# Performance work log

Measured on AMD Instinct MI355X. Metric: run time of the kernel, lower is better.

Reference implementation:

```python
import jax, jax.numpy as jnp
import numpy as np

HEADS, DH, M, ITERS = 8, 64, 256, 6
DIM = 512


def layer_norm(x, g, b, eps=1e-5):
    mu = x.mean(-1, keepdims=True)
    var = x.var(-1, keepdims=True)
    return (x - mu) / jnp.sqrt(var + eps) * g + b


def moore_penrose_pinv(x, iters=ITERS):
    abs_x = jnp.abs(x)
    col = abs_x.sum(-1)
    row = abs_x.sum(-2)
    z = jnp.swapaxes(x, -1, -2) / (jnp.max(col) * jnp.max(row))
    I = jnp.eye(x.shape[-1], dtype=x.dtype)
    for _ in range(iters):
        xz = x @ z
        z = 0.25 * z @ (13.0 * I - xz @ (15.0 * I - xz @ (7.0 * I - xz)))
    return z


def nystrom_attn(x, w_qkv, w_out, b_out, res_w):
    b, n, _ = x.shape
    pad = (M - n % M) % M
    xp = jnp.pad(x, ((0, 0), (pad, 0), (0, 0)))  # left-pad seq as in lucidrains
    npad = n + pad
    l = npad // M  # == ceil(n / M)
    qkv = xp @ w_qkv
    q, k, v = jnp.split(qkv, 3, axis=-1)
    to_heads = lambda t: t.reshape(b, npad, HEADS, DH).transpose(0, 2, 1, 3)
    q, k, v = to_heads(q), to_heads(k), to_heads(v)
    q = q * (DH ** -0.5)
    # landmarks: mean over consecutive chunks of size l  ('(n l) d -> n d')
    ql = q.reshape(b, HEADS, M, l, DH).mean(3)
    kl = k.reshape(b, HEADS, M, l, DH).mean(3)
    a1 = jax.nn.softmax(jnp.einsum('bhid,bhjd->bhij', q, kl), -1)   # (b,h,npad,M)
    a2 = jax.nn.softmax(jnp.einsum('bhid,bhjd->bhij', ql, kl), -1)  # (b,h,M,M)
    a3 = jax.nn.softmax(jnp.einsum('bhid,bhjd->bhij', ql, k), -1)   # (b,h,M,npad)
    a2inv = moore_penrose_pinv(a2)
    out = a1 @ (a2inv @ (a3 @ v))  # (b,h,npad,DH)
    # residual depthwise conv along sequence, per head (kernel (33,1), groups=heads)
    res = jax.lax.conv_general_dilated(v, res_w, window_strides=(1, 1),
                                       padding=((16, 16), (0, 0)),
                                       dimension_numbers=('NCHW', 'OIHW', 'NCHW'),
                                       feature_group_count=HEADS)
    out = out + res
    out = out.transpose(0, 2, 1, 3).reshape(b, npad, HEADS * DH)
    out = out @ w_out + b_out
    return out[:, -n:]


def ppeg(x, w7, b7, w5, b5, w3, b3, Hh, Ww):
    B, n, C = x.shape
    cls_tok, feat = x[:, :1], x[:, 1:]
    cnn = feat.transpose(0, 2, 1).reshape(B, C, Hh, Ww)

    def dwconv(w, bb, p):
        y = jax.lax.conv_general_dilated(cnn, w, (1, 1), ((p, p), (p, p)),
                                         dimension_numbers=('NCHW', 'OIHW', 'NCHW'),
                                         feature_group_count=C)
        return y + bb[None, :, None, None]

    y = cnn + dwconv(w7, b7, 3) + dwconv(w5, b5, 2) + dwconv(w3, b3, 1)
    y = y.reshape(B, C, Hh * Ww).transpose(0, 2, 1)
    return jnp.concatenate([cls_tok, y], axis=1)


def setup_inputs() -> dict:
    key = jax.random.key(0)
    ks = iter(jax.random.split(key, 32))
    rn = lambda shape, s=0.02: jax.random.normal(next(ks), shape, dtype=jnp.float32) * s
    inp = {
        'data': jax.random.normal(next(ks), (1, 16000, 1024), dtype=jnp.float32),
        'fc1_w': rn((1024, 512)), 'fc1_b': jnp.zeros((512,), jnp.float32),
        'cls_token': rn((1, 1, 512), 1.0),
        'l1_norm_g': jnp.ones((512,), jnp.float32), 'l1_norm_b': jnp.zeros((512,), jnp.float32),
        'l1_qkv_w': rn((512, 1536)), 'l1_out_w': rn((512, 512)), 'l1_out_b': jnp.zeros((512,), jnp.float32),
        'l1_res_w': rn((8, 1, 33, 1)),
        'ppeg_w7': rn((512, 1, 7, 7)), 'ppeg_b7': jnp.zeros((512,), jnp.float32),
        'ppeg_w5': rn((512, 1, 5, 5)), 'ppeg_b5': jnp.zeros((512,), jnp.float32),
        'ppeg_w3': rn((512, 1, 3, 3)), 'ppeg_b3': jnp.zeros((512,), jnp.float32),
        'l2_norm_g': jnp.ones((512,), jnp.float32), 'l2_norm_b': jnp.zeros((512,), jnp.float32),
        'l2_qkv_w': rn((512, 1536)), 'l2_out_w': rn((512, 512)), 'l2_out_b': jnp.zeros((512,), jnp.float32),
        'l2_res_w': rn((8, 1, 33, 1)),
        'norm_g': jnp.ones((512,), jnp.float32), 'norm_b': jnp.zeros((512,), jnp.float32),
        'fc2_w': rn((512, 2)), 'fc2_b': jnp.zeros((2,), jnp.float32),
    }
    return inp


def reference(data, fc1_w, fc1_b, cls_token, l1_norm_g, l1_norm_b, l1_qkv_w, l1_out_w,
              l1_out_b, l1_res_w, ppeg_w7, ppeg_b7, ppeg_w5, ppeg_b5, ppeg_w3, ppeg_b3,
              l2_norm_g, l2_norm_b, l2_qkv_w, l2_out_w, l2_out_b, l2_res_w,
              norm_g, norm_b, fc2_w, fc2_b):
    h = jax.nn.relu(data @ fc1_w + fc1_b)  # (B, N, 512)
    N = h.shape[1]
    s = int(np.ceil(np.sqrt(N)))  # square grid side
    add = s * s - N
    h = jnp.concatenate([h, h[:, :add]], axis=1)  # repeat-pad to s*s
    B = h.shape[0]
    cls = jnp.broadcast_to(cls_token, (B, 1, h.shape[2]))
    h = jnp.concatenate([cls, h], axis=1)  # (B, s*s+1, 512)
    h = h + nystrom_attn(layer_norm(h, l1_norm_g, l1_norm_b), l1_qkv_w, l1_out_w, l1_out_b, l1_res_w)
    h = ppeg(h, ppeg_w7, ppeg_b7, ppeg_w5, ppeg_b5, ppeg_w3, ppeg_b3, s, s)
    h = h + nystrom_attn(layer_norm(h, l2_norm_g, l2_norm_b), l2_qkv_w, l2_out_w, l2_out_b, l2_res_w)
    h = layer_norm(h, norm_g, norm_b)[:, 0]
    logits = h @ fc2_w + fc2_b
    Y_prob = jax.nn.softmax(logits, -1)
    Y_hat = jnp.argmax(logits, -1)
    return logits, Y_prob, Y_hat
```

## Files before the change

### kernel.cpp

```cpp
#include <hip/hip_runtime.h>
#include <math.h>

#define NPAD   16384
#define PADR   254
#define NTOK   16130
#define NPIX   16129
#define SG     127
#define DD     512
#define NH     8
#define CHK    64

typedef __attribute__((ext_vector_type(8))) short bf16x8;
typedef __attribute__((ext_vector_type(4))) float f32x4;

__device__ __forceinline__ ushort f2bf(float f) {
  uint u = __float_as_uint(f);
  u = (u + 0x7fffu + ((u >> 16) & 1u)) >> 16;
  return (ushort)u;
}

__global__ __launch_bounds__(256) void cvt_bf_kernel(
    const float* __restrict__ src, ushort* __restrict__ dst, int n)
{
  int i = (blockIdx.x * 256 + threadIdx.x) * 8;
// ... 42 lines not shown
#pragma unroll
    for (int j = 0; j < 4; ++j) acc[i][j] = (f32x4){0.f, 0.f, 0.f, 0.f};

  for (int k0 = 0; k0 < K; k0 += 64) {
    __syncthreads();
#pragma unroll
    for (int i = 0; i < 4; ++i) {
      int id = t + i * 256;
      int r = id >> 3, blk = id & 7;
      int gr = m0 + r;
      bf16x8 v = (bf16x8){0, 0, 0, 0, 0, 0, 0, 0};
      if (gr < M) v = *(const bf16x8*)(A + (size_t)gr * lda + k0 + blk * 8);
      *(bf16x8*)(As + r * 64 + ((blk ^ (r & 7)) << 3)) = v;
    }
#pragma unroll
    for (int i = 0; i < 4; ++i) {
      int id = t + i * 256;
      int r = id >> 3, blk = id & 7;
      bf16x8 v = *(const bf16x8*)(Bt + (size_t)(n0 + r) * ldb + k0 + blk * 8);
      *(bf16x8*)(Bs + r * 64 + ((blk ^ (r & 7)) << 3)) = v;
    }
    __syncthreads();
    bf16x8 af[4][2], bfr[4][2];
#pragma unroll
    for (int rt = 0; rt < 4; ++rt) {
      int row = wr * 64 + rt * 16 + lr;
#pragma unroll
      for (int kc = 0; kc < 2; ++kc)
        af[rt][kc] = *(const bf16x8*)(As + row * 64 + (((kc * 4 + lg) ^ (row & 7)) << 3));
    }
#pragma unroll
    for (int nt = 0; nt < 4; ++nt) {
      int row = wc * 64 + nt * 16 + lr;
#pragma unroll
      for (int kc = 0; kc < 2; ++kc)
        bfr[nt][kc] = *(const bf16x8*)(Bs + row * 64 + (((kc * 4 + lg) ^ (row & 7)) << 3));
    }
#pragma unroll
    for (int rt = 0; rt < 4; ++rt)
#pragma unroll
      for (int nt = 0; nt < 4; ++nt) {
        acc[rt][nt] = __builtin_amdgcn_mfma_f32_16x16x32_bf16(af[rt][0], bfr[nt][0], acc[rt][nt], 0, 0, 0);
        acc[rt][nt] = __builtin_amdgcn_mfma_f32_16x16x32_bf16(af[rt][1], bfr[nt][1], acc[rt][nt], 0, 0, 0);
      }
  }
#pragma unroll
  for (int rt = 0; rt < 4; ++rt) {
#pragma unroll
    for (int r = 0; r < 4; ++r) {
      int gi = m0 + wr * 64 + rt * 16 + lg * 4 + r;
      if (gi >= M) continue;
#pragma unroll
      for (int nt = 0; nt < 4; ++nt) {
        int gj = n0 + wc * 64 + nt * 16 + lr;
        float d = acc[rt][nt][r];
        if (mode == 1) d = fmaxf(d + bias[gj], 0.f);
        else if (mode == 2) { if (gj < 512) d *= 0.125f; }
        else if (mode == 3) d += C[(size_t)gi * ldc + gj] + bias[gj];
        C[(size_t)gi * ldc + gj] = d;
      }
    }
  }
}

__global__ __launch_bounds__(256) void gemm_bt(
    const float* __restrict__ A, int lda,
    const ushort* __restrict__ Bt, int ldb,
    float* __restrict__ C, int ldc,
    int M, int K, int mode, const float* __restrict__ bias)
{
  const int t = threadIdx.x;
  const int w = t >> 6, l = t & 63, lr = l & 15, lg = l >> 4;
  const int wr = w >> 1, wc = w & 1;
  const int m0 = blockIdx.y * 128, n0 = blockIdx.x * 128;
  __shared__ __align__(16) ushort As[128 * 64];
  __shared__ __align__(16) ushort Bs[128 * 64];
  f32x4 acc[4][4];
#pragma unroll
  for (int i = 0; i < 4; ++i)
#pragma unroll
    for (int j = 0; j < 4; ++j) acc[i][j] = (f32x4){0.f, 0.f, 0.f, 0.f};

  for (int k0 = 0; k0 < K; k0 += 64) {
    __syncthreads();
#pragma unroll
    for (int i = 0; i < 2; ++i) {
      int id = t + i * 256;
      int r = id >> 2, db = id & 3;
      const float* src = A + (size_t)(m0 + r) * lda + k0 + db * 16;
      float4 g0 = *(const float4*)(src + 0);
      float4 g1 = *(const float4*)(src + 4);
      float4 g2 = *(const float4*)(src + 8);
      float4 g3 = *(const float4*)(src + 12);
      bf16x8 e0, e1;
      e0[0] = f2bf(g0.x); e0[1] = f2bf(g0.y); e0[2] = f2bf(g0.z); e0[3] = f2bf(g0.w);
      e0[4] = f2bf(g1.x); e0[5] = f2bf(g1.y); e0[6] = f2bf(g1.z); e0[7] = f2bf(g1.w);
      e1[0] = f2bf(g2.x); e1[1] = f2bf(g2.y); e1[2] = f2bf(g2.z); e1[3] = f2bf(g2.w);
      e1[4] = f2bf(g3.x); e1[5] = f2bf(g3.y); e1[6] = f2bf(g3.z); e1[7] = f2bf(g3.w);
      ushort* dst = As + r * 64;
      *(bf16x8*)(dst + (((db * 2 + 0) ^ (r & 7)) << 3)) = e0;
      *(bf16x8*)(dst + (((db * 2 + 1) ^ (r & 7)) << 3)) = e1;
    }
#pragma unroll
    for (int i = 0; i < 4; ++i) {
      int id = t + i * 256;
      int r = id >> 3, blk = id & 7;
      bf16x8 v = *(const bf16x8*)(Bt + (size_t)(n0 + r) * ldb + k0 + blk * 8);
      *(bf16x8*)(Bs + r * 64 + ((blk ^ (r & 7)) << 3)) = v;
    }
    __syncthreads();
    bf16x8 af[4][2], bfr[4][2];
#pragma unroll
    for (int rt = 0; rt < 4; ++rt) {
      int row = wr * 64 + rt * 16 + lr;
#pragma unroll
      for (int kc = 0; kc < 2; ++kc)
        af[rt][kc] = *(const bf16x8*)(As + row * 64 + (((kc * 4 + lg) ^ (row & 7)) << 3));
    }
#pragma unroll
    for (int nt = 0; nt < 4; ++nt) {
      int row = wc * 64 + nt * 16 + lr;
#pragma unroll
      for (int kc = 0; kc < 2; ++kc)
        bfr[nt][kc] = *(const bf16x8*)(Bs + row * 64 + (((kc * 4 + lg) ^ (row & 7)) << 3));
    }
#pragma unroll
    for (int rt = 0; rt < 4; ++rt)
#pragma unroll
      for (int nt = 0; nt < 4; ++nt) {
        acc[rt][nt] = __builtin_amdgcn_mfma_f32_16x16x32_bf16(af[rt][0], bfr[nt][0], acc[rt][nt], 0, 0, 0);
        acc[rt][nt] = __builtin_amdgcn_mfma_f32_16x16x32_bf16(af[rt][1], bfr[nt][1], acc[rt][nt], 0, 0, 0);
      }
  }
#pragma unroll
  for (int rt = 0; rt < 4; ++rt) {
#pragma unroll
    for (int r = 0; r < 4; ++r) {
      int gi = m0 + wr * 64 + rt * 16 + lg * 4 + r;
      if (gi >= M) continue;
#pragma unroll
      for (int nt = 0; nt < 4; ++nt) {
        int gj = n0 + wc * 64 + nt * 16 + lr;
        float d = acc[rt][nt][r];
        if (mode == 1) d = fmaxf(d + bias[gj], 0.f);
        else if (mode == 2) { if (gj < 512) d *= 0.125f; }
        else if (mode == 3) d += C[(size_t)gi * ldc + gj] + bias[gj];
        C[(size_t)gi * ldc + gj] = d;
      }
    }
  }
}


__global__ __launch_bounds__(256) void nmm_kernel(
    const float* __restrict__ A, const float* __restrict__ B,
    float* __restrict__ C, int mode)
{
  const int h_ = blockIdx.z;
  const int m0 = blockIdx.y * 64, n0 = blockIdx.x * 64;
  const float* Ah = A + (size_t)h_ * 65536;
  const float* Bh = B + (size_t)h_ * 65536;
  float* Ch = C + (size_t)h_ * 65536;
  const int t = threadIdx.x, w = t >> 6, l = t & 63, lr = l & 15, lg = l >> 4;
  __shared__ __align__(16) ushort Xs[64 * 64];
  __shared__ __align__(16) ushort Ys[64 * 64];
  f32x4 acc[4];
#pragma unroll
  for (int nt = 0; nt < 4; ++nt) acc[nt] = (f32x4){0.f, 0.f, 0.f, 0.f};

  for (int k0 = 0; k0 < 256; k0 += 64) {
    __syncthreads();
    {
      int r = t >> 2, db = t & 3;
      const float* src = Ah + (size_t)(m0 + r) * 256 + k0 + db * 16;
      float4 g0 = *(const float4*)(src + 0);
      float4 g1 = *(const float4*)(src + 4);
      float4 g2 = *(const float4*)(src + 8);
      float4 g3 = *(const float4*)(src + 12);
      bf16x8 e0, e1;
      e0[0] = f2bf(g0.x); e0[1] = f2bf(g0.y); e0[2] = f2bf(g0.z); e0[3] = f2bf(g0.w);
      e0[4] = f2bf(g1.x); e0[5] = f2bf(g1.y); e0[6] = f2bf(g1.z); e0[7] = f2bf(g1.w);
      e1[0] = f2bf(g2.x); e1[1] = f2bf(g2.y); e1[2] = f2bf(g2.z); e1[3] = f2bf(g2.w);
      e1[4] = f2bf(g3.x); e1[5] = f2bf(g3.y); e1[6] = f2bf(g3.z); e1[7] = f2bf(g3.w);
      ushort* dst = Xs + r * 64;
      *(bf16x8*)(dst + (((db * 2 + 0) ^ (r & 7)) << 3)) = e0;
      *(bf16x8*)(dst + (((db * 2 + 1) ^ (r & 7)) << 3)) = e1;
    }
#pragma unroll
    for (int i = 0; i < 4; ++i) {
      int id = t + i * 256;
      int k = id >> 4, q = id & 15;
      float4 v = *(const float4*)(Bh + (size_t)(k0 + k) * 256 + n0 + q * 4);
      int kb = k >> 3, ke = k & 7;
      Ys[(q * 4 + 0) * 64 + ((kb ^ ((q * 4 + 0) & 7)) << 3) + ke] = f2bf(v.x);
      Ys[(q * 4 + 1) * 64 + ((kb ^ ((q * 4 + 1) & 7)) << 3) + ke] = f2bf(v.y);
      Ys[(q * 4 + 2) * 64 + ((kb ^ ((q * 4 + 2) & 7)) << 3) + ke] = f2bf(v.z);
      Ys[(q * 4 + 3) * 64 + ((kb ^ ((q * 4 + 3) & 7)) << 3) + ke] = f2bf(v.w);
    }
    __syncthreads();
    int arow = w * 16 + lr;
    bf16x8 af0 = *(const bf16x8*)(Xs + arow * 64 + (((0 + lg) ^ (arow & 7)) << 3));
    bf16x8 af1 = *(const bf16x8*)(Xs + arow * 64 + (((4 + lg) ^ (arow & 7)) << 3));
#pragma unroll
    for (int nt = 0; nt < 4; ++nt) {
      int brow = nt * 16 + lr;
      bf16x8 bf0 = *(const bf16x8*)(Ys + brow * 64 + (((0 + lg) ^ (brow & 7)) << 3));
      bf16x8 bf1 = *(const bf16x8*)(Ys + brow * 64 + (((4 + lg) ^ (brow & 7)) << 3));
      acc[nt] = __builtin_amdgcn_mfma_f32_16x16x32_bf16(af0, bf0, acc[nt], 0, 0, 0);
      acc[nt] = __builtin_amdgcn_mfma_f32_16x16x32_bf16(af1, bf1, acc[nt], 0, 0, 0);
    }
  }
#pragma unroll
  for (int nt = 0; nt < 4; ++nt) {
#pragma unroll
    for (int r = 0; r < 4; ++r) {
      int gi = m0 + w * 16 + lg * 4 + r;
      int gj = n0 + nt * 16 + lr;
      float d = acc[nt][r];
      if (mode == 1) d = 7.f * Ah[(size_t)gi * 256 + gj] - d;
      Ch[(size_t)gi * 256 + gj] = d;
    }
  }
}

__global__ __launch_bounds__(256) void nmm_s2(
    const float* __restrict__ Z, const float* __restrict__ z,
    float* __restrict__ W, float* __restrict__ G)
{
  const int h_ = blockIdx.z & 7;
  const int job = blockIdx.z >> 3;
  const int m0 = blockIdx.y * 64, n0 = blockIdx.x * 64;
  const float* Ah = Z + (size_t)h_ * 65536;
  const float* Bh = (job == 0 ? z : Z) + (size_t)h_ * 65536;
  float* Ch = (job == 0 ? W : G) + (size_t)h_ * 65536;
  const int t = threadIdx.x, w = t >> 6, l = t & 63, lr = l & 15, lg = l >> 4;
  __shared__ __align__(16) ushort Xs[64 * 64];
  __shared__ __align__(16) ushort Ys[64 * 64];
  f32x4 acc[4];
#pragma unroll
  for (int nt = 0; nt < 4; ++nt) acc[nt] = (f32x4){0.f, 0.f, 0.f, 0.f};

  for (int k0 = 0; k0 < 256; k0 += 64) {
    __syncthreads();
    {
      int r = t >> 2, db = t & 3;
      const float* src = Ah + (size_t)(m0 + r) * 256 + k0 + db * 16;
      float4 g0 = *(const float4*)(src + 0);
      float4 g1 = *(const float4*)(src + 4);
      float4 g2 = *(const float4*)(src + 8);
      float4 g3 = *(const float4*)(src + 12);
      bf16x8 e0, e1;
      e0[0] = f2bf(g0.x); e0[1] = f2bf(g0.y); e0[2] = f2bf(g0.z); e0[3] = f2bf(g0.w);
      e0[4] = f2bf(g1.x); e0[5] = f2bf(g1.y); e0[6] = f2bf(g1.z); e0[7] = f2bf(g1.w);
      e1[0] = f2bf(g2.x); e1[1] = f2bf(g2.y); e1[2] = f2bf(g2.z); e1[3] = f2bf(g2.w);
      e1[4] = f2bf(g3.x); e1[5] = f2bf(g3.y); e1[6] = f2bf(g3.z); e1[7] = f2bf(g3.w);
      ushort* dst = Xs + r * 64;
      *(bf16x8*)(dst + (((db * 2 + 0) ^ (r & 7)) << 3)) = e0;
      *(bf16x8*)(dst + (((db * 2 + 1) ^ (r & 7)) << 3)) = e1;
    }
#pragma unroll
    for (int i = 0; i < 4; ++i) {
      int id = t + i * 256;
      int k = id >> 4, q = id & 15;
      float4 v = *(const float4*)(Bh + (size_t)(k0 + k) * 256 + n0 + q * 4);
      int kb = k >> 3, ke = k & 7;
      Ys[(q * 4 + 0) * 64 + ((kb ^ ((q * 4 + 0) & 7)) << 3) + ke] = f2bf(v.x);
      Ys[(q * 4 + 1) * 64 + ((kb ^ ((q * 4 + 1) & 7)) << 3) + ke] = f2bf(v.y);
      Ys[(q * 4 + 2) * 64 + ((kb ^ ((q * 4 + 2) & 7)) << 3) + ke] = f2bf(v.z);
      Ys[(q * 4 + 3) * 64 + ((kb ^ ((q * 4 + 3) & 7)) << 3) + ke] = f2bf(v.w);
    }
    __syncthreads();
    int arow = w * 16 + lr;
    bf16x8 af0 = *(const bf16x8*)(Xs + arow * 64 + (((0 + lg) ^ (arow & 7)) << 3));
    bf16x8 af1 = *(const bf16x8*)(Xs + arow * 64 + (((4 + lg) ^ (arow & 7)) << 3));
#pragma unroll
    for (int nt = 0; nt < 4; ++nt) {
      int brow = nt * 16 + lr;
      bf16x8 bf0 = *(const bf16x8*)(Ys + brow * 64 + (((0 + lg) ^ (brow & 7)) << 3));
      bf16x8 bf1 = *(const bf16x8*)(Ys + brow * 64 + (((4 + lg) ^ (brow & 7)) << 3));
      acc[nt] = __builtin_amdgcn_mfma_f32_16x16x32_bf16(af0, bf0, acc[nt], 0, 0, 0);
      acc[nt] = __builtin_amdgcn_mfma_f32_16x16x32_bf16(af1, bf1, acc[nt], 0, 0, 0);
    }
  }
#pragma unroll
  for (int nt = 0; nt < 4; ++nt) {
#pragma unroll
    for (int r = 0; r < 4; ++r) {
      int gi = m0 + w * 16 + lg * 4 + r;
      int gj = n0 + nt * 16 + lr;
      float d = acc[nt][r];
      if (job == 1) d = 7.f * Ah[(size_t)gi * 256 + gj] - d;
      Ch[(size_t)gi * 256 + gj] = d;
    }
  }
}

__global__ __launch_bounds__(256) void nmm_s3(
    const float* __restrict__ G, const float* __restrict__ W,
    const float* __restrict__ zc, float* __restrict__ zn)
{
  const int h_ = blockIdx.z;
  const int m0 = blockIdx.y * 64, n0 = blockIdx.x * 64;
  const float* Ah = G + (size_t)h_ * 65536;
  const float* Bh = W + (size_t)h_ * 65536;
  const float* Eh = zc + (size_t)h_ * 65536;
  float* Ch = zn + (size_t)h_ * 65536;
  const int t = threadIdx.x, w = t >> 6, l = t & 63, lr = l & 15, lg = l >> 4;
  __shared__ __align__(16) ushort Xs[64 * 64];
  __shared__ __align__(16) ushort Ys[64 * 64];
  f32x4 acc[4];
#pragma unroll
  for (int nt = 0; nt < 4; ++nt) acc[nt] = (f32x4){0.f, 0.f, 0.f, 0.f};

  for (int k0 = 0; k0 < 256; k0 += 64) {
    __syncthreads();
    {
      int r = t >> 2, db = t & 3;
      const float* src = Ah + (size_t)(m0 + r) * 256 + k0 + db * 16;
      float4 g0 = *(const float4*)(src + 0);
      float4 g1 = *(const float4*)(src + 4);
      float4 g2 = *(const float4*)(src + 8);
      float4 g3 = *(const float4*)(src + 12);
      bf16x8 e0, e1;
      e0[0] = f2bf(g0.x); e0[1] = f2bf(g0.y); e0[2] = f2bf(g0.z); e0[3] = f2bf(g0.w);
      e0[4] = f2bf(g1.x); e0[5] = f2bf(g1.y); e0[6] = f2bf(g1.z); e0[7] = f2bf(g1.w);
      e1[0] = f2bf(g2.x); e1[1] = f2bf(g2.y); e1[2] = f2bf(g2.z); e1[3] = f2bf(g2.w);
      e1[4] = f2bf(g3.x); e1[5] = f2bf(g3.y); e1[6] = f2bf(g3.z); e1[7] = f2bf(g3.w);
      ushort* dst = Xs + r * 64;
      *(bf16x8*)(dst + (((db * 2 + 0) ^ (r & 7)) << 3)) = e0;
      *(bf16x8*)(dst + (((db * 2 + 1) ^ (r & 7)) << 3)) = e1;
    }
#pragma unroll
    for (int i = 0; i < 4; ++i) {
      int id = t + i * 256;
      int k = id >> 4, q = id & 15;
      float4 v = *(const float4*)(Bh + (size_t)(k0 + k) * 256 + n0 + q * 4);
      int kb = k >> 3, ke = k & 7;
      Ys[(q * 4 + 0) * 64 + ((kb ^ ((q * 4 + 0) & 7)) << 3) + ke] = f2bf(v.x);
      Ys[(q * 4 + 1) * 64 + ((kb ^ ((q * 4 + 1) & 7)) << 3) + ke] = f2bf(v.y);
      Ys[(q * 4 + 2) * 64 + ((kb ^ ((q * 4 + 2) & 7)) << 3) + ke] = f2bf(v.z);
      Ys[(q * 4 + 3) * 64 + ((kb ^ ((q * 4 + 3) & 7)) << 3) + ke] = f2bf(v.w);
    }
    __syncthreads();
    int arow = w * 16 + lr;
    bf16x8 af0 = *(const bf16x8*)(Xs + arow * 64 + (((0 + lg) ^ (arow & 7)) << 3));
    bf16x8 af1 = *(const bf16x8*)(Xs + arow * 64 + (((4 + lg) ^ (arow & 7)) << 3));
#pragma unroll
    for (int nt = 0; nt < 4; ++nt) {
      int brow = nt * 16 + lr;
      bf16x8 bf0 = *(const bf16x8*)(Ys + brow * 64 + (((0 + lg) ^ (brow & 7)) << 3));
      bf16x8 bf1 = *(const bf16x8*)(Ys + brow * 64 + (((4 + lg) ^ (brow & 7)) << 3));
      acc[nt] = __builtin_amdgcn_mfma_f32_16x16x32_bf16(af0, bf0, acc[nt], 0, 0, 0);
      acc[nt] = __builtin_amdgcn_mfma_f32_16x16x32_bf16(af1, bf1, acc[nt], 0, 0, 0);
    }
  }
#pragma unroll
  for (int nt = 0; nt < 4; ++nt) {
#pragma unroll
    for (int r = 0; r < 4; ++r) {
      int gi = m0 + w * 16 + lg * 4 + r;
      int gj = n0 + nt * 16 + lr;
      size_t o = (size_t)gi * 256 + gj;
      Ch[o] = 0.25f * (13.f * Eh[o] - 15.f * Bh[o] + acc[nt][r]);
    }
  }
}

__global__ __launch_bounds__(256) void assemble_kernel(float* __restrict__ h,
                                                       const float* __restrict__ cls)
{
  int idx = blockIdx.x * 256 + threadIdx.x;
  if (idx < 512) { h[idx] = cls[idx]; return; }
  idx -= 512;
  int i = idx >> 9, c = idx & 511;
  h[(size_t)(16001 + i) * DD + c] = h[(size_t)(1 + i) * DD + c];
}

__global__ __launch_bounds__(256) void ln_pad_kernel(
    const float* __restrict__ h, ushort* __restrict__ xn,
    const float* __restrict__ g, const float* __restrict__ b)
{
  int row = blockIdx.x;
  int t = threadIdx.x;
  if (row < PADR) {
    xn[(size_t)row * DD + t] = 0;
    xn[(size_t)row * DD + t + 256] = 0;
    return;
  }
  const float* x = h + (size_t)(row - PADR) * DD;
  __shared__ float red[256];
  float v0 = x[t], v1 = x[t + 256];
  red[t] = v0 + v1;
  __syncthreads();
  for (int s = 128; s > 0; s >>= 1) { if (t < s) red[t] += red[t + s]; __syncthreads(); }
  float mu = red[0] * (1.f / 512.f);
  __syncthreads();
  float d0 = v0 - mu, d1 = v1 - mu;
  red[t] = d0 * d0 + d1 * d1;
  __syncthreads();
  for (int s = 128; s > 0; s >>= 1) { if (t < s) red[t] += red[t + s]; __syncthreads(); }
  float rs = rsqrtf(red[0] * (1.f / 512.f) + 1e-5f);
  ushort* o = xn + (size_t)row * DD;
  o[t]       = f2bf(d0 * rs * g[t] + b[t]);
  o[t + 256] = f2bf(d1 * rs * g[t + 256] + b[t + 256]);
}

__global__ __launch_bounds__(256) void landmark_kernel(
    const float* __restrict__ qkv, float* __restrict__ ql, float* __restrict__ kl)
{
  int i = blockIdx.x;
  int c = blockIdx.y * 256 + threadIdx.x;
  const float* p = qkv + (size_t)(i * 64) * 1536 + c;
  float s = 0.f;
  for (int j = 0; j < 64; ++j) s += p[(size_t)j * 1536];
  s *= (1.f / 64.f);
  if (c < 512) ql[(size_t)i * 512 + c] = s;
  else         kl[(size_t)i * 512 + (c - 512)] = s;
}

__global__ __launch_bounds__(256) void a2_kernel(
    const float* __restrict__ ql, const float* __restrict__ kl, float* __restrict__ a2)
{
  int h_ = blockIdx.x, i = blockIdx.y;
  int t = threadIdx.x;
  __shared__ float q[64];
  __shared__ float red[256];
  if (t < 64) q[t] = ql[(size_t)i * 512 + h_ * 64 + t];
  __syncthreads();
  const float* kr = kl + (size_t)t * 512 + h_ * 64;
  float s = 0.f;
#pragma unroll
  for (int d = 0; d < 64; ++d) s = fmaf(q[d], kr[d], s);
  red[t] = s;
  __syncthreads();
  for (int st = 128; st > 0; st >>= 1) { if (t < st) red[t] = fmaxf(red[t], red[t + st]); __syncthreads(); }
  float mx = red[0];
  __syncthreads();
  float e = __expf(s - mx);
  red[t] = e;
  __syncthreads();
  for (int st = 128; st > 0; st >>= 1) { if (t < st) red[t] += red[t + st]; __syncthreads(); }
  a2[((size_t)h_ * 256 + i) * 256 + t] = e / red[0];
}

__global__ __launch_bounds__(256) void pinv_red1(const float* __restrict__ a2, float* __restrict__ red)
{
  int h_ = blockIdx.x, t = threadIdx.x;
  const float* X = a2 + (size_t)h_ * 65536;
  float rs = 0.f, cs = 0.f;
  for (int j = 0; j < 256; ++j) rs += fabsf(X[(size_t)t * 256 + j]);
  for (int i = 0; i < 256; ++i) cs += fabsf(X[(size_t)i * 256 + t]);
  __shared__ float r1[256], r2[256];
  r1[t] = rs; r2[t] = cs;
  __syncthreads();
  for (int s = 128; s > 0; s >>= 1) {
    if (t < s) { r1[t] = fmaxf(r1[t], r1[t + s]); r2[t] = fmaxf(r2[t], r2[t + s]); }
    __syncthreads();
  }
  if (t == 0) { red[h_ * 2] = r1[0]; red[h_ * 2 + 1] = r2[0]; }
}
__global__ __launch_bounds__(256) void pinv_init(
    const float* __restrict__ a2, const float* __restrict__ red, float* __restrict__ z)
{
  int h_ = blockIdx.x, i = blockIdx.y, j = threadIdx.x;
  float mr = 0.f, mc = 0.f;
#pragma unroll
  for (int k = 0; k < 8; ++k) { mr = fmaxf(mr, red[k * 2]); mc = fmaxf(mc, red[k * 2 + 1]); }
  float inv = 1.f / (mr * mc);
  z[((size_t)h_ * 256 + i) * 256 + j] = a2[((size_t)h_ * 256 + j) * 256 + i] * inv;
}

__global__ __launch_bounds__(256) void mmb_kernel(
    const float* __restrict__ A, const float* __restrict__ B, float* __restrict__ C,
    int N, float alpha)
{
  int h_ = blockIdx.z;
  const float* Ah = A + (size_t)h_ * 256 * 256;
  const float* Bh = B + (size_t)h_ * 256 * N;
  float* Ch = C + (size_t)h_ * 256 * N;
  int m0 = blockIdx.y * 64, n0 = blockIdx.x * 64;
  __shared__ float As[16][68];
  __shared__ float Bs[16][68];
  int tid = threadIdx.x, tx = tid & 15, ty = tid >> 4;
  float acc[4][4];
#pragma unroll
  for (int i = 0; i < 4; ++i)
#pragma unroll
    for (int j = 0; j < 4; ++j) acc[i][j] = 0.f;
  for (int k0 = 0; k0 < 256; k0 += 16) {
    {
      int row = tid >> 2, k4 = (tid & 3) << 2;
      float4 v = *(const float4*)(Ah + (size_t)(m0 + row) * 256 + k0 + k4);
      As[k4 + 0][row] = v.x; As[k4 + 1][row] = v.y;
      As[k4 + 2][row] = v.z; As[k4 + 3][row] = v.w;
    }
    {
      int row = tid >> 4, c4 = (tid & 15) << 2;
      *(float4*)&Bs[row][c4] = *(const float4*)(Bh + (size_t)(k0 + row) * N + n0 + c4);
    }
    __syncthreads();
#pragma unroll
    for (int k = 0; k < 16; ++k) {
      float a[4], b[4];
      *(float4*)a = *(const float4*)&As[k][ty * 4];
      *(float4*)b = *(const float4*)&Bs[k][tx * 4];
#pragma unroll
      for (int i = 0; i < 4; ++i)
#pragma unroll
        for (int j = 0; j < 4; ++j) acc[i][j] = fmaf(a[i], b[j], acc[i][j]);
    }
    __syncthreads();
  }
#pragma unroll
  for (int i = 0; i < 4; ++i) {
    float4 r;
    r.x = alpha * acc[i][0]; r.y = alpha * acc[i][1];
    r.z = alpha * acc[i][2]; r.w = alpha * acc[i][3];
    *(float4*)(Ch + (size_t)(m0 + ty * 4 + i) * N + n0 + tx * 4) = r;
  }
}

__global__ __launch_bounds__(256) void a3v_mfma(
    const float* __restrict__ qkv, const float* __restrict__ ql,
    float* __restrict__ pacc, float* __restrict__ den)
{
  const int h_ = blockIdx.x;
  const int ch = blockIdx.y;
  const int t  = threadIdx.x;
  const int w  = t >> 6;
  const int l  = t & 63;
  const int lr = l & 15;
  const int lg = l >> 4;

  __shared__ __align__(16) ushort kls[64 * 64];
  __shared__ __align__(16) ushort vls[80 * 64];
  __shared__ __align__(16) ushort pls[4][64 * 64];

  bf16x8 qf[4][2];
#pragma unroll
  for (int rt = 0; rt < 4; ++rt)
#pragma unroll
    for (int dc = 0; dc < 2; ++dc) {
      const float* p = ql + (size_t)(64 * w + rt * 16 + lr) * 512 + h_ * 64 + dc * 32 + lg * 8;
      float4 f0 = *(const float4*)p;
      float4 f1 = *(const float4*)(p + 4);
      bf16x8 v;
      v[0] = f2bf(f0.x); v[1] = f2bf(f0.y); v[2] = f2bf(f0.z); v[3] = f2bf(f0.w);
      v[4] = f2bf(f1.x); v[5] = f2bf(f1.y); v[6] = f2bf(f1.z); v[7] = f2bf(f1.w);
      qf[rt][dc] = v;
    }

  if (t < 128) {
    int rr = t >> 3, cb = t & 7;
    ushort val = (rr == 0) ? (ushort)0x3f80 : (ushort)0;
    bf16x8 vv;
#pragma unroll
    for (int k = 0; k < 8; ++k) vv[k] = (short)val;
    *(bf16x8*)(vls + (64 + rr) * 64 + ((cb ^ (rr & 7)) << 3)) = vv;
  }

  f32x4 acc[4][5];
#pragma unroll
  for (int rt = 0; rt < 4; ++rt)
#pragma unroll
    for (int dt = 0; dt < 5; ++dt) acc[rt][dt] = (f32x4){0.f, 0.f, 0.f, 0.f};

  const int j0base = ch * 256;
  for (int jt = 0; jt < 4; ++jt) {
    const int j0 = j0base + jt * 64;
    __syncthreads();
    {
      int r = t >> 2, db = t & 3;
      const float* src = qkv + (size_t)(j0 + r) * 1536 + 512 + h_ * 64 + db * 16;
      float4 g0 = *(const float4*)(src + 0);
      float4 g1 = *(const float4*)(src + 4);
      float4 g2 = *(const float4*)(src + 8);
      float4 g3 = *(const float4*)(src + 12);
      bf16x8 e0, e1;
      e0[0] = f2bf(g0.x); e0[1] = f2bf(g0.y); e0[2] = f2bf(g0.z); e0[3] = f2bf(g0.w);
      e0[4] = f2bf(g1.x); e0[5] = f2bf(g1.y); e0[6] = f2bf(g1.z); e0[7] = f2bf(g1.w);
      e1[0] = f2bf(g2.x); e1[1] = f2bf(g2.y); e1[2] = f2bf(g2.z); e1[3] = f2bf(g2.w);
      e1[4] = f2bf(g3.x); e1[5] = f2bf(g3.y); e1[6] = f2bf(g3.z); e1[7] = f2bf(g3.w);
      ushort* base = kls + r * 64;
      *(bf16x8*)(base + (((db * 2 + 0) ^ (r & 7)) << 3)) = e0;
      *(bf16x8*)(base + (((db * 2 + 1) ^ (r & 7)) << 3)) = e1;
    }
    {
      int d = t & 63, jg = t >> 6;
#pragma unroll
      for (int half = 0; half < 2; ++half) {
        int jb = jg + half * 4;
        bf16x8 e;
#pragma unroll
        for (int jj = 0; jj < 8; ++jj)
          e[jj] = f2bf(qkv[(size_t)(j0 + jb * 8 + jj) * 1536 + 1024 + h_ * 64 + d]);
        *(bf16x8*)(vls + d * 64 + ((jb ^ (d & 7)) << 3)) = e;
      }
    }
    __syncthreads();

    ushort* pw = pls[w];
#pragma unroll
    for (int sjt = 0; sjt < 4; ++sjt) {
      const int krow = sjt * 16 + lr;
      bf16x8 kf0 = *(const bf16x8*)(kls + krow * 64 + (((0 * 4 + lg) ^ (lr & 7)) << 3));
      bf16x8 kf1 = *(const bf16x8*)(kls + krow * 64 + (((1 * 4 + lg) ^ (lr & 7)) << 3));
#pragma unroll
      for (int rt = 0; rt < 4; ++rt) {
        f32x4 s = (f32x4){0.f, 0.f, 0.f, 0.f};
        s = __builtin_amdgcn_mfma_f32_16x16x32_bf16(qf[rt][0], kf0, s, 0, 0, 0);
        s = __builtin_amdgcn_mfma_f32_16x16x32_bf16(qf[rt][1], kf1, s, 0, 0, 0);
#pragma unroll
        for (int r = 0; r < 4; ++r) {
          int i  = rt * 16 + lg * 4 + r;
          int jj = sjt * 16 + lr;
          pw[i * 64 + ((((jj >> 3) ^ (i & 7)) << 3)) + (jj & 7)] = (short)f2bf(__expf(s[r]));
        }
      }
    }
    bf16x8 pf[4][2];
#pragma unroll
    for (int rt = 0; rt < 4; ++rt)
// ... 243 lines not shown
                   ? h[(size_t)(1 + yy * SG + xx) * DD + c] : 0.f;
    }
  }

#pragma unroll 1
  for (int j = 0; j < 14; ++j) {
    float vnext[7];
    if (j < 13) {
      int xx = x0 + j - 2;
      bool okx = (xx >= 0 && xx < SG);
#pragma unroll
      for (int ky = 0; ky < 7; ++ky) {
        int yy = y + ky - 3;
        vnext[ky] = (okx && yy >= 0 && yy < SG)
                      ? h[(size_t)(1 + yy * SG + xx) * DD + c] : 0.f;
      }
    }
#pragma unroll
    for (int i = 0; i < 8; ++i) {
      const int k7 = j - i;
      if (k7 >= 0 && k7 <= 6) {
        const float* w7p = wl + k7 * 64 + tc;
#pragma unroll
        for (int ky = 0; ky < 7; ++ky)
          acc[i] = fmaf(vcur[ky], w7p[ky * 7 * 64], acc[i]);
      }
      const int k5 = j - i - 1;
      if (k5 >= 0 && k5 <= 4) {
        const float* w5p = wl + (49 + k5) * 64 + tc;
#pragma unroll
        for (int ky = 0; ky < 5; ++ky)
          acc[i] = fmaf(vcur[ky + 1], w5p[ky * 5 * 64], acc[i]);
      }
      const int k3 = j - i - 2;
      if (k3 >= 0 && k3 <= 2) {
        const float* w3p = wl + (74 + k3) * 64 + tc;
#pragma unroll
        for (int ky = 0; ky < 3; ++ky)
          acc[i] = fmaf(vcur[ky + 2], w3p[ky * 3 * 64], acc[i]);
      }
    }
    if (j < 13) {
#pragma unroll
      for (int ky = 0; ky < 7; ++ky) vcur[ky] = vnext[ky];
    }
  }
#pragma unroll
  for (int i = 0; i < 8; ++i) {
    int x = x0 + i;
    if (x < SG) {
      int p = y * SG + x;
      tmp[(size_t)p * DD + c] = h[(size_t)(1 + p) * DD + c] + bsum + acc[i];
    }
  }
}

__global__ __launch_bounds__(256) void final_kernel(
    const float* __restrict__ h, const float* __restrict__ g, const float* __restrict__ b,
    const float* __restrict__ w, const float* __restrict__ bias, float* __restrict__ out)
{
  __shared__ float red[256];
  int t = threadIdx.x;
  float v0 = h[t], v1 = h[t + 256];
  red[t] = v0 + v1;
  __syncthreads();
  for (int s = 128; s > 0; s >>= 1) { if (t < s) red[t] += red[t + s]; __syncthreads(); }
  float mu = red[0] * (1.f / 512.f);
  __syncthreads();
  float d0 = v0 - mu, d1 = v1 - mu;
  red[t] = d0 * d0 + d1 * d1;
  __syncthreads();
  for (int s = 128; s > 0; s >>= 1) { if (t < s) red[t] += red[t + s]; __syncthreads(); }
  float rs = rsqrtf(red[0] * (1.f / 512.f) + 1e-5f);
  __syncthreads();
  float x0 = d0 * rs * g[t] + b[t];
  float x1 = d1 * rs * g[t + 256] + b[t + 256];
  red[t] = x0 * w[t * 2] + x1 * w[(t + 256) * 2];
  __syncthreads();
  for (int s = 128; s > 0; s >>= 1) { if (t < s) red[t] += red[t + s]; __syncthreads(); }
  float l0 = red[0] + bias[0];
  __syncthreads();
  red[t] = x0 * w[t * 2 + 1] + x1 * w[(t + 256) * 2 + 1];
  __syncthreads();
  for (int s = 128; s > 0; s >>= 1) { if (t < s) red[t] += red[t + s]; __syncthreads(); }
  float l1 = red[0] + bias[1];
  if (t == 0) {
    out[0] = l0; out[1] = l1;
    float mx = fmaxf(l0, l1);
    float e0 = __expf(l0 - mx), e1 = __expf(l1 - mx);
    float inv = 1.f / (e0 + e1);
    out[2] = e0 * inv; out[3] = e1 * inv;
    out[4] = (l1 > l0) ? 1.f : 0.f;
  }
}

extern "C" void kernel_launch(void* const* d_in, const int* in_sizes, int n_in,
                              void* d_out, int out_size, void* d_ws, size_t ws_size,
                              hipStream_t stream)
{
  const float* data   = (const float*)d_in[0];
  const float* fc1_w  = (const float*)d_in[1];
  const float* fc1_b  = (const float*)d_in[2];
  const float* cls    = (const float*)d_in[3];
  const float* l1_g   = (const float*)d_in[4];
  const float* l1_b   = (const float*)d_in[5];
  const float* l1_qkv = (const float*)d_in[6];
  const float* l1_ow  = (const float*)d_in[7];
  const float* l1_ob  = (const float*)d_in[8];
  const float* l1_rw  = (const float*)d_in[9];
  const float* w7     = (const float*)d_in[10];
  const float* b7     = (const float*)d_in[11];
  const float* w5     = (const float*)d_in[12];
  const float* b5     = (const float*)d_in[13];
  const float* w3     = (const float*)d_in[14];
  const float* b3     = (const float*)d_in[15];
  const float* l2_g   = (const float*)d_in[16];
  const float* l2_b   = (const float*)d_in[17];
  const float* l2_qkv = (const float*)d_in[18];
  const float* l2_ow  = (const float*)d_in[19];
  const float* l2_ob  = (const float*)d_in[20];
  const float* l2_rw  = (const float*)d_in[21];
  const float* ng     = (const float*)d_in[22];
  const float* nb     = (const float*)d_in[23];
  const float* fc2_w  = (const float*)d_in[24];
  const float* fc2_b  = (const float*)d_in[25];
  float* out = (float*)d_out;

  float* ws   = (float*)d_ws;
  float* h    = ws;
  float* xn   = h    + (size_t)16384 * 512;
  float* qkv  = xn   + (size_t)16384 * 512;
  float* attn = qkv  + (size_t)16384 * 1536;
  float* ql   = attn + (size_t)16384 * 512;
  float* kl   = ql   + 256 * 512;
  float* a2b  = kl   + 256 * 512;
  float* z0   = a2b  + 8 * 256 * 256;
  float* z1   = z0   + 8 * 256 * 256;
  float* xzb  = z1   + 8 * 256 * 256;
  float* tb   = xzb  + 8 * 256 * 256;
  float* ub   = tb   + 8 * 256 * 256;
  float* a3v  = ub   + 8 * 256 * 256;
  float* w2   = a3v  + 8 * 256 * 64;
  float* pacc = w2   + 8 * 256 * 64;
  float* pms  = pacc + (size_t)8 * 32 * 256 * 64;
  float* red  = pms  + (size_t)8 * 32 * 256 * 2;
  float* wtb  = red  + 32;

  ushort* fc1_wt  = (ushort*)pacc;
  ushort* qkv_wt0 = fc1_wt + 512 * 1024;
  ushort* qkv_wt1 = qkv_wt0 + 1536 * 512;
  ushort* out_wt0 = qkv_wt1 + 1536 * 512;
  ushort* out_wt1 = out_wt0 + 512 * 512;

  ushort* xnb    = (ushort*)xn;
  ushort* databf = (ushort*)qkv;

  float* a3v_pacc = xn;
  float* a3v_den  = pms;

  wtrans_bf<<<dim3(16, 32), 256, 0, stream>>>(fc1_w, fc1_wt, 1024, 512);
  wtrans_bf<<<dim3(48, 16), 256, 0, stream>>>(l1_qkv, qkv_wt0, 512, 1536);
  wtrans_bf<<<dim3(48, 16), 256, 0, stream>>>(l2_qkv, qkv_wt1, 512, 1536);
  wtrans_bf<<<dim3(16, 16), 256, 0, stream>>>(l1_ow, out_wt0, 512, 512);
  wtrans_bf<<<dim3(16, 16), 256, 0, stream>>>(l2_ow, out_wt1, 512, 512);
  wtrans_kernel<<<2, 256, 0, stream>>>(w7, w5, w3, wtb);
  cvt_bf_kernel<<<8000, 256, 0, stream>>>(data, databf, 16000 * 1024);

  gemm_bb<<<dim3(4, 125), 256, 0, stream>>>(databf, 1024, fc1_wt, 1024, h + 512, 512,
                                            16000, 1024, 1, fc1_b);
  assemble_kernel<<<260, 256, 0, stream>>>(h, cls);

  for (int layer = 0; layer < 2; ++layer) {
    const float* gg = layer ? l2_g   : l1_g;
    const float* bb = layer ? l2_b   : l1_b;
    const ushort* qw = layer ? qkv_wt1 : qkv_wt0;
    const ushort* ow = layer ? out_wt1 : out_wt0;
    const float* ob = layer ? l2_ob  : l1_ob;
    const float* rw = layer ? l2_rw  : l1_rw;

    ln_pad_kernel<<<16384, 256, 0, stream>>>(h, xnb, gg, bb);
    gemm_bb<<<dim3(12, 128), 256, 0, stream>>>(xnb, 512, qw, 512, qkv, 1536,
                                               16384, 512, 2, nullptr);
    landmark_kernel<<<dim3(256, 4), 256, 0, stream>>>(qkv, ql, kl);
    a2_kernel<<<dim3(8, 256), 256, 0, stream>>>(ql, kl, a2b);
    pinv_red1<<<8, 256, 0, stream>>>(a2b, red);
    pinv_init<<<dim3(8, 256), 256, 0, stream>>>(a2b, red, z0);
    float* zc = z0; float* zn = z1;
    for (int it = 0; it < 6; ++it) {
      nmm_kernel<<<dim3(4, 4, 8), 256, 0, stream>>>(zc, a2b, xzb, 0);
      nmm_s2<<<dim3(4, 4, 16), 256, 0, stream>>>(xzb, zc, tb, ub);
      nmm_s3<<<dim3(4, 4, 8), 256, 0, stream>>>(ub, tb, zc, zn);
      float* sw = zc; zc = zn; zn = sw;
    }
    a3v_mfma<<<dim3(8, CHK), 256, 0, stream>>>(qkv, ql, a3v_pacc, a3v_den);
    a3v_merge_kernel<<<dim3(8, 256), 64, 0, stream>>>(a3v_pacc, a3v_den, a3v);
    mmb_kernel<<<dim3(1, 4, 8), 256, 0, stream>>>(zc, a3v, w2, 64, 1.f);
    a1_mfma<<<dim3(8, 64), 256, 0, stream>>>(qkv, kl, w2, attn);
    resconv_kernel<<<dim3(2048, 2), 256, 0, stream>>>(qkv, rw, attn);
    gemm_bt<<<dim3(4, 127), 256, 0, stream>>>(attn + (size_t)254 * 512, 512, ow, 512,
                                              h, 512, 16130, 512, 3, ob);
    if (layer == 0) {
      ppeg_kernel<<<dim3(127 * 4, 8), 256, 0, stream>>>(h, qkv, wtb, b7, b5, b3);
      hipMemcpyAsync(h + 512, qkv, (size_t)16129 * 512 * 4,
                     hipMemcpyDeviceToDevice, stream);
    }
  }
  final_kernel<<<1, 256, 0, stream>>>(h, ng, nb, fc2_w, fc2_b, out);
}
```

Measured before the change: 1.097 ms.

## Restructure Newton-Schulz pinv iteration to track Y=A·Z, cutting kernels per iteration

Reformulates the Moore-Penrose iteration to carry both Z and Y = Z·A (seeded by a new pinv_seed kernel that builds z0 and its product with a2). Each iteration now runs two batched GEMM launches instead of three, and the 7I-XZ correction is fused into the operand load of the second stage. This removes a serial kernel launch and one dependent matmul stage per iteration. In exchange it computes an extra matmul for the Y update, and the bf16 rounding now accumulates in Y as well as Z.

```diff
diff --git a/kernel.cpp b/kernel.cpp
--- a/kernel.cpp
+++ b/kernel.cpp
@@ -218,15 +218,19 @@
 }
 
 
-__global__ __launch_bounds__(256) void nmm_kernel(
-    const float* __restrict__ A, const float* __restrict__ B,
-    float* __restrict__ C, int mode)
+__global__ __launch_bounds__(256) void pinv_seed(
+    const float* __restrict__ a2, const float* __restrict__ red,
+    float* __restrict__ z0, float* __restrict__ Y0)
 {
   const int h_ = blockIdx.z;
   const int m0 = blockIdx.y * 64, n0 = blockIdx.x * 64;
-  const float* Ah = A + (size_t)h_ * 65536;
-  const float* Bh = B + (size_t)h_ * 65536;
-  float* Ch = C + (size_t)h_ * 65536;
+  const float* Ah = a2 + (size_t)h_ * 65536;
+  float* zh = z0 + (size_t)h_ * 65536;
+  float* Yh = Y0 + (size_t)h_ * 65536;
+  float mr = 0.f, mc = 0.f;
+#pragma unroll
+  for (int k = 0; k < 8; ++k) { mr = fmaxf(mr, red[k * 2]); mc = fmaxf(mc, red[k * 2 + 1]); }
+  const float inv = 1.f / (mr * mc);
   const int t = threadIdx.x, w = t >> 6, l = t & 63, lr = l & 15, lg = l >> 4;
   __shared__ __align__(16) ushort Xs[64 * 64];
   __shared__ __align__(16) ushort Ys[64 * 64];
@@ -252,16 +256,21 @@
       *(bf16x8*)(dst + (((db * 2 + 0) ^ (r & 7)) << 3)) = e0;
       *(bf16x8*)(dst + (((db * 2 + 1) ^ (r & 7)) << 3)) = e1;
     }
-#pragma unroll
-    for (int i = 0; i < 4; ++i) {
-      int id = t + i * 256;
-      int k = id >> 4, q = id & 15;
-      float4 v = *(const float4*)(Bh + (size_t)(k0 + k) * 256 + n0 + q * 4);
-      int kb = k >> 3, ke = k & 7;
-      Ys[(q * 4 + 0) * 64 + ((kb ^ ((q * 4 + 0) & 7)) << 3) + ke] = f2bf(v.x);
-      Ys[(q * 4 + 1) * 64 + ((kb ^ ((q * 4 + 1) & 7)) << 3) + ke] = f2bf(v.y);
-      Ys[(q * 4 + 2) * 64 + ((kb ^ ((q * 4 + 2) & 7)) << 3) + ke] = f2bf(v.z);
-      Ys[(q * 4 + 3) * 64 + ((kb ^ ((q * 4 + 3) & 7)) << 3) + ke] = f2bf(v.w);
+    {
+      int r = t >> 2, db = t & 3;
+      const float* src = Ah + (size_t)(n0 + r) * 256 + k0 + db * 16;
+      float4 g0 = *(const float4*)(src + 0);
+      float4 g1 = *(const float4*)(src + 4);
+      float4 g2 = *(const float4*)(src + 8);
+      float4 g3 = *(const float4*)(src + 12);
+      bf16x8 e0, e1;
+      e0[0] = f2bf(g0.x); e0[1] = f2bf(g0.y); e0[2] = f2bf(g0.z); e0[3] = f2bf(g0.w);
+      e0[4] = f2bf(g1.x); e0[5] = f2bf(g1.y); e0[6] = f2bf(g1.z); e0[7] = f2bf(g1.w);
+      e1[0] = f2bf(g2.x); e1[1] = f2bf(g2.y); e1[2] = f2bf(g2.z); e1[3] = f2bf(g2.w);
+      e1[4] = f2bf(g3.x); e1[5] = f2bf(g3.y); e1[6] = f2bf(g3.z); e1[7] = f2bf(g3.w);
+      ushort* dst = Ys + r * 64;
+      *(bf16x8*)(dst + (((db * 2 + 0) ^ (r & 7)) << 3)) = e0;
+      *(bf16x8*)(dst + (((db * 2 + 1) ^ (r & 7)) << 3)) = e1;
     }
     __syncthreads();
     int arow = w * 16 + lr;
@@ -282,23 +291,27 @@
     for (int r = 0; r < 4; ++r) {
       int gi = m0 + w * 16 + lg * 4 + r;
       int gj = n0 + nt * 16 + lr;
-      float d = acc[nt][r];
-      if (mode == 1) d = 7.f * Ah[(size_t)gi * 256 + gj] - d;
-      Ch[(size_t)gi * 256 + gj] = d;
-    }
-  }
-}
-
-__global__ __launch_bounds__(256) void nmm_s2(
-    const float* __restrict__ Z, const float* __restrict__ z,
-    float* __restrict__ W, float* __restrict__ G)
+      Yh[(size_t)gi * 256 + gj] = inv * acc[nt][r];
+    }
+  }
+#pragma unroll
+  for (int e = 0; e < 16; ++e) {
+    int id = e * 256 + t;
+    int i = id >> 6, j = id & 63;
+    zh[(size_t)(m0 + i) * 256 + n0 + j] = inv * Ah[(size_t)(n0 + j) * 256 + m0 + i];
+  }
+}
+
+__global__ __launch_bounds__(256) void nmm_A(
+    const float* __restrict__ z, const float* __restrict__ Y,
+    float* __restrict__ U, float* __restrict__ Y2)
 {
   const int h_ = blockIdx.z & 7;
   const int job = blockIdx.z >> 3;
   const int m0 = blockIdx.y * 64, n0 = blockIdx.x * 64;
-  const float* Ah = Z + (size_t)h_ * 65536;
-  const float* Bh = (job == 0 ? z : Z) + (size_t)h_ * 65536;
-  float* Ch = (job == 0 ? W : G) + (size_t)h_ * 65536;
+  const float* Ah = (job == 0 ? z : Y) + (size_t)h_ * 65536;
+  const float* Bh = Y + (size_t)h_ * 65536;
+  float* Ch = (job == 0 ? U : Y2) + (size_t)h_ * 65536;
   const int t = threadIdx.x, w = t >> 6, l = t & 63, lr = l & 15, lg = l >> 4;
   __shared__ __align__(16) ushort Xs[64 * 64];
   __shared__ __align__(16) ushort Ys[64 * 64];
@@ -354,23 +367,23 @@
     for (int r = 0; r < 4; ++r) {
       int gi = m0 + w * 16 + lg * 4 + r;
       int gj = n0 + nt * 16 + lr;
-      float d = acc[nt][r];
-      if (job == 1) d = 7.f * Ah[(size_t)gi * 256 + gj] - d;
-      Ch[(size_t)gi * 256 + gj] = d;
-    }
-  }
-}
-
-__global__ __launch_bounds__(256) void nmm_s3(
-    const float* __restrict__ G, const float* __restrict__ W,
-    const float* __restrict__ zc, float* __restrict__ zn)
-{
-  const int h_ = blockIdx.z;
+      Ch[(size_t)gi * 256 + gj] = acc[nt][r];
+    }
+  }
+}
+
+__global__ __launch_bounds__(256) void nmm_B(
+    const float* __restrict__ z, const float* __restrict__ Y,
+    const float* __restrict__ U, const float* __restrict__ Y2,
+    float* __restrict__ zn, float* __restrict__ yn)
+{
+  const int h_ = blockIdx.z & 7;
+  const int job = blockIdx.z >> 3;
   const int m0 = blockIdx.y * 64, n0 = blockIdx.x * 64;
-  const float* Ah = G + (size_t)h_ * 65536;
-  const float* Bh = W + (size_t)h_ * 65536;
-  const float* Eh = zc + (size_t)h_ * 65536;
-  float* Ch = zn + (size_t)h_ * 65536;
+  const float* X1 = (job == 0 ? z : Y) + (size_t)h_ * 65536;
+  const float* X2 = (job == 0 ? U : Y2) + (size_t)h_ * 65536;
+  const float* Bh = Y2 + (size_t)h_ * 65536;
+  float* Ch = (job == 0 ? zn : yn) + (size_t)h_ * 65536;
   const int t = threadIdx.x, w = t >> 6, l = t & 63, lr = l & 15, lg = l >> 4;
   __shared__ __align__(16) ushort Xs[64 * 64];
   __shared__ __align__(16) ushort Ys[64 * 64];
@@ -382,16 +395,21 @@
     __syncthreads();
     {
       int r = t >> 2, db = t & 3;
-      const float* src = Ah + (size_t)(m0 + r) * 256 + k0 + db * 16;
-      float4 g0 = *(const float4*)(src + 0);
-      float4 g1 = *(const float4*)(src + 4);
-      float4 g2 = *(const float4*)(src + 8);
-      float4 g3 = *(const float4*)(src + 12);
+      const float* s1 = X1 + (size_t)(m0 + r) * 256 + k0 + db * 16;
+      const float* s2 = X2 + (size_t)(m0 + r) * 256 + k0 + db * 16;
+      float4 a0 = *(const float4*)(s1 + 0),  b0 = *(const float4*)(s2 + 0);
+      float4 a1 = *(const float4*)(s1 + 4),  b1 = *(const float4*)(s2 + 4);
+      float4 a2v = *(const float4*)(s1 + 8), b2 = *(const float4*)(s2 + 8);
+      float4 a3 = *(const float4*)(s1 + 12), b3 = *(const float4*)(s2 + 12);
       bf16x8 e0, e1;
-      e0[0] = f2bf(g0.x); e0[1] = f2bf(g0.y); e0[2] = f2bf(g0.z); e0[3] = f2bf(g0.w);
-      e0[4] = f2bf(g1.x); e0[5] = f2bf(g1.y); e0[6] = f2bf(g1.z); e0[7] = f2bf(g1.w);
-      e1[0] = f2bf(g2.x); e1[1] = f2bf(g2.y); e1[2] = f2bf(g2.z); e1[3] = f2bf(g2.w);
-      e1[4] = f2bf(g3.x); e1[5] = f2bf(g3.y); e1[6] = f2bf(g3.z); e1[7] = f2bf(g3.w);
+      e0[0] = f2bf(7.f * a0.x - b0.x); e0[1] = f2bf(7.f * a0.y - b0.y);
+      e0[2] = f2bf(7.f * a0.z - b0.z); e0[3] = f2bf(7.f * a0.w - b0.w);
+      e0[4] = f2bf(7.f * a1.x - b1.x); e0[5] = f2bf(7.f * a1.y - b1.y);
+      e0[6] = f2bf(7.f * a1.z - b1.z); e0[7] = f2bf(7.f * a1.w - b1.w);
+      e1[0] = f2bf(7.f * a2v.x - b2.x); e1[1] = f2bf(7.f * a2v.y - b2.y);
+      e1[2] = f2bf(7.f * a2v.z - b2.z); e1[3] = f2bf(7.f * a2v.w - b2.w);
+      e1[4] = f2bf(7.f * a3.x - b3.x); e1[5] = f2bf(7.f * a3.y - b3.y);
+      e1[6] = f2bf(7.f * a3.z - b3.z); e1[7] = f2bf(7.f * a3.w - b3.w);
       ushort* dst = Xs + r * 64;
       *(bf16x8*)(dst + (((db * 2 + 0) ^ (r & 7)) << 3)) = e0;
       *(bf16x8*)(dst + (((db * 2 + 1) ^ (r & 7)) << 3)) = e1;
@@ -427,7 +445,7 @@
       int gi = m0 + w * 16 + lg * 4 + r;
       int gj = n0 + nt * 16 + lr;
       size_t o = (size_t)gi * 256 + gj;
-      Ch[o] = 0.25f * (13.f * Eh[o] - 15.f * Bh[o] + acc[nt][r]);
+      Ch[o] = 0.25f * (13.f * X1[o] - 15.f * X2[o] + acc[nt][r]);
     }
   }
 }
@@ -524,16 +542,6 @@
     __syncthreads();
   }
   if (t == 0) { red[h_ * 2] = r1[0]; red[h_ * 2 + 1] = r2[0]; }
-}
-__global__ __launch_bounds__(256) void pinv_init(
-    const float* __restrict__ a2, const float* __restrict__ red, float* __restrict__ z)
-{
-  int h_ = blockIdx.x, i = blockIdx.y, j = threadIdx.x;
-  float mr = 0.f, mc = 0.f;
-#pragma unroll
-  for (int k = 0; k < 8; ++k) { mr = fmaxf(mr, red[k * 2]); mc = fmaxf(mc, red[k * 2 + 1]); }
-  float inv = 1.f / (mr * mc);
-  z[((size_t)h_ * 256 + i) * 256 + j] = a2[((size_t)h_ * 256 + j) * 256 + i] * inv;
 }
 
 __global__ __launch_bounds__(256) void mmb_kernel(
@@ -1083,6 +1091,9 @@
   ushort* out_wt0 = qkv_wt1 + 1536 * 512;
   ushort* out_wt1 = out_wt0 + 512 * 512;
 
+  float* yb0 = pacc + 1310720;
+  float* yb1 = yb0 + 8 * 256 * 256;
+
   ushort* xnb    = (ushort*)xn;
   ushort* databf = (ushort*)qkv;
 
@@ -1115,13 +1126,13 @@
     landmark_kernel<<<dim3(256, 4), 256, 0, stream>>>(qkv, ql, kl);
     a2_kernel<<<dim3(8, 256), 256, 0, stream>>>(ql, kl, a2b);
     pinv_red1<<<8, 256, 0, stream>>>(a2b, red);
-    pinv_init<<<dim3(8, 256), 256, 0, stream>>>(a2b, red, z0);
-    float* zc = z0; float* zn = z1;
+    pinv_seed<<<dim3(4, 4, 8), 256, 0, stream>>>(a2b, red, z0, yb0);
+    float* zc = z0; float* zn = z1; float* yc = yb0; float* yn = yb1;
     for (int it = 0; it < 6; ++it) {
-      nmm_kernel<<<dim3(4, 4, 8), 256, 0, stream>>>(zc, a2b, xzb, 0);
-      nmm_s2<<<dim3(4, 4, 16), 256, 0, stream>>>(xzb, zc, tb, ub);
-      nmm_s3<<<dim3(4, 4, 8), 256, 0, stream>>>(ub, tb, zc, zn);
-      float* sw = zc; zc = zn; zn = sw;
+      nmm_A<<<dim3(4, 4, 16), 256, 0, stream>>>(zc, yc, ub, tb);
+      nmm_B<<<dim3(4, 4, 16), 256, 0, stream>>>(zc, yc, ub, tb, zn, yn);
+      float* s = zc; zc = zn; zn = s;
+      s = yc; yc = yn; yn = s;
     }
     a3v_mfma<<<dim3(8, CHK), 256, 0, stream>>>(qkv, ql, a3v_pacc, a3v_den);
     a3v_merge_kernel<<<dim3(8, 256), 64, 0, stream>>>(a3v_pacc, a3v_den, a3v);
```

Result: faster. 946.7 us (-13.7%).
